# Performance work log

Hardware: AMD Instinct MI355X
Metric: run time of the kernel (lower is better)

Reference implementation:

```python
import jax, jax.numpy as jnp
import numpy as np

KS = 5          # B-spline kernel_size per pseudo-coordinate dim
DIM = 2         # pseudo-coordinate dimensionality
NUM_GRAPHS = 64


def spline_conv(x, src, dst, edge_attr, W, root, bias):
    """Degree-1 open B-spline conv (torch-spline-conv semantics, aggr='mean').
    x: [N,Cin], edge_attr: [E,DIM] in [0,1], W: [KS**DIM,Cin,Cout]."""
    N = x.shape[0]
    E = src.shape[0]
    v = edge_attr * (KS - 1)                                   # [E,DIM]
    k_lo = jnp.clip(jnp.floor(v), 0, KS - 2).astype(jnp.int32) # lower knot index
    frac = v - k_lo.astype(v.dtype)                            # [E,DIM]
    # Precompute x @ W_k for all K kernel weights per node: [N,K,Cout]
    xW = jnp.einsum('nc,kco->nko', x, W)
    msg = jnp.zeros((E, W.shape[2]), x.dtype)
    # 2^DIM = 4 nonzero basis products for degree-1 splines
    for bits in ((0, 0), (0, 1), (1, 0), (1, 1)):
        b = jnp.ones((E,), x.dtype)
        wi = jnp.zeros((E,), jnp.int32)
        stride = 1
        for d, bit in enumerate(bits):
            b = b * (frac[:, d] if bit else (1.0 - frac[:, d]))
            wi = wi + (k_lo[:, d] + bit) * stride
            stride *= KS
        msg = msg + b[:, None] * xW[src, wi]                   # gather [E,Cout]
    agg = jax.ops.segment_sum(msg, dst, num_segments=N)
    deg = jax.ops.segment_sum(jnp.ones((E,), x.dtype), dst, num_segments=N)
    agg = agg / jnp.maximum(deg, 1.0)[:, None]                 # mean aggregation
    return agg + x @ root + bias


def setup_inputs() -> dict:
    key = jax.random.key(0)
    ks = jax.random.split(key, 12)
    N, E = 20000, 320000
    Cin, H, O = 1, 32, 10
    K = KS * KS
    p = lambda k, s: jax.random.normal(k, s, jnp.float32) * 0.1
    return {
        'x': jax.random.normal(ks[0], (N, Cin), jnp.float32),
        'edge_attr': jax.random.uniform(ks[1], (E, DIM), jnp.float32),
        'W1': p(ks[2], (K, Cin, H)), 'root1': p(ks[3], (Cin, H)), 'b1': jnp.zeros((H,), jnp.float32),
        'W2': p(ks[4], (K, H, 2 * H)), 'root2': p(ks[5], (H, 2 * H)), 'b2': jnp.zeros((2 * H,), jnp.float32),
        'Wf1': p(ks[6], (2 * H, 128)), 'bf1': jnp.zeros((128,), jnp.float32),
        'Wf2': p(ks[7], (128, O)), 'bf2': jnp.zeros((O,), jnp.float32),
        'edge_index': jax.random.randint(ks[8], (2, E), 0, N),
        'batch': jnp.sort(jax.random.randint(ks[9], (N,), 0, NUM_GRAPHS)),
    }


def reference(x, edge_attr, W1, root1, b1, W2, root2, b2, Wf1, bf1, Wf2, bf2, edge_index, batch):
    src, dst = edge_index[0], edge_index[1]
    h = jax.nn.relu(spline_conv(x, src, dst, edge_attr, W1, root1, b1))
    h = jax.nn.relu(spline_conv(h, src, dst, edge_attr, W2, root2, b2))
    # global mean pool over graphs
    gsum = jax.ops.segment_sum(h, batch, num_segments=NUM_GRAPHS)
    cnt = jax.ops.segment_sum(jnp.ones((h.shape[0],), h.dtype), batch, num_segments=NUM_GRAPHS)
    g = gsum / jnp.maximum(cnt, 1.0)[:, None]
    g = jax.nn.relu(g @ Wf1 + bf1)
    return jax.nn.log_softmax(g @ Wf2 + bf2, axis=1)
```

## Files before the change

kernel.cpp:

```cpp
#include <hip/hip_runtime.h>
#include <hip/hip_fp16.h>
#include <math.h>

#define KK 25
#define H1C 32
#define H2C 64
#define FCC 128
#define NCLS 10
#define NG 64
#define M1 16
#define M2 10
#define TILEU 12800

typedef _Float16 v8h __attribute__((ext_vector_type(8)));
typedef _Float16 v4h __attribute__((ext_vector_type(4)));
typedef float v4f __attribute__((ext_vector_type(4)));

__global__ __launch_bounds__(256) void deg_kernel(
    const int* __restrict__ edge_index, int E,
    int* __restrict__ degi,
    const float* __restrict__ W2, __half* __restrict__ W2t) {
    int i = blockIdx.x * 256 + threadIdx.x;
    if (i < KK * H2C * H1C) {
        int c = i & 31, o = (i >> 5) & 63, k = i >> 11;
        W2t[i] = __float2half(W2[(k * H1C + c) * H2C + o]);
    }
    if (i < E) atomicAdd(&degi[edge_index[E + i]], 1);
}

__global__ void scan1_kernel(const int* __restrict__ degi, int N,
                             int* __restrict__ incl, int* __restrict__ bsum) {
    __shared__ int s[256];
    int tid = threadIdx.x;
    int i = blockIdx.x * 256 + tid;
    int v = (i < N) ? degi[i] : 0;
    s[tid] = v;
    __syncthreads();
    for (int off = 1; off < 256; off <<= 1) {
        int t = (tid >= off) ? s[tid - off] : 0;
        __syncthreads();
        s[tid] += t;
        __syncthreads();
    }
    if (i < N) incl[i] = s[tid];
    if (tid == 255) bsum[blockIdx.x] = s[255];
}

__global__ void scan23_kernel(const int* __restrict__ incl, const int* __restrict__ degi,
                              const int* __restrict__ bsum, int nb, int N,
                              int* __restrict__ rowst, int* __restrict__ cur) {
    __shared__ int s[256];
    int tid = threadIdx.x;
    int lim = min(nb, (int)blockIdx.x);
    int v = 0;
    for (int j = tid; j < lim; j += 256) v += bsum[j];
    s[tid] = v;
    __syncthreads();
    for (int off = 1; off < 256; off <<= 1) {
        int t = (tid >= off) ? s[tid - off] : 0;
        __syncthreads();
        s[tid] += t;
        __syncthreads();
    }
    int prior = s[255];
    int i = blockIdx.x * 256 + tid;
    if (i < N) {
        int r = incl[i] - degi[i] + prior;
        rowst[i] = r;
        cur[i] = r;
    }
}

__global__ void bucket_kernel(const float* __restrict__ edge_attr,
                              const int* __restrict__ edge_index, int E,
                              int* __restrict__ cur, int4* __restrict__ es) {
    int e = blockIdx.x * blockDim.x + threadIdx.x;
    if (e >= E) return;
    float v0 = edge_attr[2 * e + 0] * 4.0f;
    float v1 = edge_attr[2 * e + 1] * 4.0f;
    int k0 = (int)floorf(v0); k0 = min(max(k0, 0), 3);
    int k1 = (int)floorf(v1); k1 = min(max(k1, 0), 3);
    float f0 = v0 - (float)k0, f1 = v1 - (float)k1;
    int dst = edge_index[E + e];
    int pos = atomicAdd(&cur[dst], 1);
    es[pos] = make_int4(edge_index[e], (dst << 8) | (k0 + 5 * k1),
                        __float_as_int(f0), __float_as_int(f1));
}

__global__ __launch_bounds__(256) void l1_kernel(
    const float* __restrict__ x,
    const int* __restrict__ rowst, const int* __restrict__ degi,
    const int4* __restrict__ es,
    const float* __restrict__ W1, const float* __restrict__ root1,
    const float* __restrict__ b1,
    const __half* __restrict__ W2t,
    int N, int E,
    float* __restrict__ h1, __half* __restrict__ xph) {
    __shared__ float w1s[KK * H1C];
    __shared__ float agg1[M1 * H1C];
    __shared__ int4 eb[8][32];
    __shared__ float xb[8][32];
    __shared__ __half h1s[M1][H1C];
    __shared__ __half stg[5][M1][68];
    int tid = threadIdx.x;
    for (int i = tid; i < KK * H1C; i += 256) w1s[i] = W1[i];
    for (int i = tid; i < M1 * H1C; i += 256) agg1[i] = 0.0f;
    __syncthreads();
    int g = tid >> 5, o = tid & 31;
    int n0 = blockIdx.x * M1;
    int blkBeg = rowst[n0];
    int blkEnd = (n0 + M1 < N) ? rowst[n0 + M1] : E;
    int total = blkEnd - blkBeg;
    int per = (total + 7) >> 3;
    int wBeg = blkBeg + g * per;
    int wEnd = min(blkEnd, wBeg + per);
    int curDst = -1;
    float acc = 0.0f;
    for (int base = wBeg; base < wEnd; base += 32) {
        int m = min(32, wEnd - base);
        if (o < m) {
            int4 ed = es[base + o];
            eb[g][o] = ed;
            xb[g][o] = x[ed.x];
        }
        for (int j = 0; j < m; j++) {
            int4 ed = eb[g][j];
            float xs = xb[g][j];
            int dst = ed.y >> 8;
            if (dst != curDst) {
                if (curDst >= 0) atomicAdd(&agg1[(curDst - n0) * H1C + o], acc);
                acc = 0.0f;
                curDst = dst;
            }
            float f0 = __int_as_float(ed.z), f1 = __int_as_float(ed.w);
            float g0 = 1.0f - f0, g1 = 1.0f - f1;
            int kb = (ed.y & 0xff) << 5;
            float coef = g0 * g1 * w1s[kb + o] + f0 * g1 * w1s[kb + 32 + o] +
                         g0 * f1 * w1s[kb + 160 + o] + f0 * f1 * w1s[kb + 192 + o];
            acc = fmaf(xs, coef, acc);
        }
    }
    if (curDst >= 0) atomicAdd(&agg1[(curDst - n0) * H1C + o], acc);
    __syncthreads();
#pragma unroll
    for (int i = 0; i < 2; i++) {
        int ln = g + 8 * i;
        int n = n0 + ln;
        if (n < N) {
            float rdeg = 1.0f / fmaxf((float)degi[n], 1.0f);
            float hv = fmaxf(agg1[ln * H1C + o] * rdeg + x[n] * root1[o] + b1[o], 0.0f);
            h1[n * H1C + o] = hv;
            h1s[ln][o] = __float2half(hv);
        } else {
            h1s[ln][o] = __float2half(0.0f);
        }
    }
    __syncthreads();

    int w = tid >> 6, lane = tid & 63;
    int r15 = lane & 15, quad = lane >> 4;
    int o0 = w * 16;
    v8h bfrag = *(const v8h*)(&h1s[r15][quad * 8]);
    __half* xtile = xph + (size_t)blockIdx.x * (2 * TILEU);
    int cln = tid >> 4, coc = (tid & 15) * 4;
    bool crow = (n0 + cln) < N;
    for (int kc = 0; kc < KK; kc += 5) {
#pragma unroll
        for (int kk = 0; kk < 5; kk++) {
            int k = kc + kk;
            v8h afrag = *(const v8h*)(W2t + ((k << 6) + o0 + r15) * H1C + quad * 8);
            v4f acc2 = {};
            acc2 = __builtin_amdgcn_mfma_f32_16x16x32_f16(afrag, bfrag, acc2, 0, 0, 0);
            v4h hv;
            hv[0] = (_Float16)acc2[0];
            hv[1] = (_Float16)acc2[1];
            hv[2] = (_Float16)acc2[2];
            hv[3] = (_Float16)acc2[3];
            *(v4h*)(&stg[kk][r15][o0 + quad * 4]) = hv;
        }
        __syncthreads();
#pragma unroll
        for (int kk = 0; kk < 5; kk++) {
            if (crow) {
                v4h hv = *(const v4h*)(&stg[kk][cln][coc]);
                *(v4h*)(xtile + ((kc + kk) << 10) + (tid << 2)) = hv;
            }
        }
        __syncthreads();
    }
}

__global__ __launch_bounds__(256) void l2_kernel(
    const float* __restrict__ h1,
    const int* __restrict__ rowst, const int* __restrict__ degi,
    const int4* __restrict__ es,
    const unsigned* __restrict__ xphu,
    const float* __restrict__ root2, const float* __restrict__ b2,
    const int* __restrict__ batch,
    int N, int E, float* __restrict__ gsum) {
    __shared__ float agg[M2 * H2C];
    __shared__ int4 eb[4][64];
    int tid = threadIdx.x;
    for (int i = tid; i < M2 * H2C; i += 256) agg[i] = 0.0f;
    __syncthreads();
    int w = tid >> 6, lane = tid & 63;
    int o2 = lane & 31, eh = lane >> 5;
    int n0 = blockIdx.x * M2;
    int blkBeg = rowst[n0];
    int blkEnd = (n0 + M2 < N) ? rowst[n0 + M2] : E;
    int total = blkEnd - blkBeg;
    int per = (total + 3) >> 2;
    int wBeg = blkBeg + w * per;
    int wEnd = min(blkEnd, wBeg + per);
    int curDst = -1;
    float ax = 0.0f, ay = 0.0f;
    for (int base = wBeg; base < wEnd; base += 64) {
        int m = min(64, wEnd - base);
        if (lane < m) eb[w][lane] = es[base + lane];
        for (int j = 0; j < m; j += 2) {
            int jj = j + eh;
            bool act = jj < m;
            int4 ed = eb[w][act ? jj : j];
            const unsigned* p = xphu + (size_t)(ed.x >> 4) * TILEU +
                                ((ed.y & 0xff) << 9) + ((ed.x & 15) << 5) + o2;
            unsigned t0 = p[0], t1 = p[512], t2 = p[2560], t3 = p[3072];
            if (act) {
                int dst = ed.y >> 8;
                if (dst != curDst) {
                    if (curDst >= 0) {
                        atomicAdd(&agg[(curDst - n0) * H2C + 2 * o2], ax);
                        atomicAdd(&agg[(curDst - n0) * H2C + 2 * o2 + 1], ay);
                    }
                    ax = ay = 0.0f;
                    curDst = dst;
                }
                float f0 = __int_as_float(ed.z), f1 = __int_as_float(ed.w);
                float g0 = 1.0f - f0, g1 = 1.0f - f1;
                float b0 = g0 * g1, b1 = f0 * g1, bb2 = g0 * f1, b3 = f0 * f1;
                __half2 h0 = *(__half2*)&t0, h1v = *(__half2*)&t1;
                __half2 h2 = *(__half2*)&t2, h3 = *(__half2*)&t3;
                ax = fmaf(b0, __low2float(h0), ax);  ay = fmaf(b0, __high2float(h0), ay);
                ax = fmaf(b1, __low2float(h1v), ax); ay = fmaf(b1, __high2float(h1v), ay);
                ax = fmaf(bb2, __low2float(h2), ax); ay = fmaf(bb2, __high2float(h2), ay);
                ax = fmaf(b3, __low2float(h3), ax);  ay = fmaf(b3, __high2float(h3), ay);
            }
        }
    }
    if (curDst >= 0) {
        atomicAdd(&agg[(curDst - n0) * H2C + 2 * o2], ax);
        atomicAdd(&agg[(curDst - n0) * H2C + 2 * o2 + 1], ay);
    }
    __syncthreads();

#pragma unroll
    for (int i = 0; i < 3; i++) {
        int ln = w + 4 * i;
        int n = n0 + ln;
        if (ln < M2) {
            if (n < N) {
                float rd = 1.0f / fmaxf((float)degi[n], 1.0f);
                float v = agg[ln * H2C + lane] * rd + b2[lane];
                const float* hr = h1 + n * H1C;
#pragma unroll 8
                for (int c = 0; c < H1C; c++) v = fmaf(hr[c], root2[c * H2C + lane], v);
                agg[ln * H2C + lane] = fmaxf(v, 0.0f);
            } else {
                agg[ln * H2C + lane] = 0.0f;
            }
        }
    }
    __syncthreads();

    if (tid < H2C) {
        float run = 0.0f;
        int curg = batch[n0];
        for (int ln = 0; ln < M2; ln++) {
            int n = n0 + ln;
            if (n >= N) break;
            int gg = batch[n];
            if (gg != curg) {
                atomicAdd(&gsum[curg * H2C + tid], run);
                run = 0.0f;
                curg = gg;
            }
            run += agg[ln * H2C + tid];
        }
        atomicAdd(&gsum[curg * H2C + tid], run);
    }
}

__global__ void head_kernel(const float* __restrict__ gsum,
                            const int* __restrict__ batch, int N,
                            const float* __restrict__ Wf1, const float* __restrict__ bf1,
                            const float* __restrict__ Wf2, const float* __restrict__ bf2,
                            float* __restrict__ out) {
    __shared__ float gc[H2C];
    __shared__ float t1[FCC];
    __shared__ float lg[NCLS];
    __shared__ float lse;
    __shared__ float scnt;
    int g = blockIdx.x, tid = threadIdx.x;
    if (tid == 0) {
        int lo = 0, hi = N;
        while (lo < hi) { int m = (lo + hi) >> 1; if (batch[m] < g) lo = m + 1; else hi = m; }
        int lb = lo;
        lo = 0; hi = N;
        while (lo < hi) { int m = (lo + hi) >> 1; if (batch[m] <= g) lo = m + 1; else hi = m; }
        scnt = (float)(lo - lb);
    }
    __syncthreads();
    if (tid < H2C) gc[tid] = gsum[g * H2C + tid] / fmaxf(scnt, 1.0f);
    __syncthreads();
    {
        float acc = bf1[tid];
        for (int c = 0; c < H2C; c++) acc += gc[c] * Wf1[c * FCC + tid];
        t1[tid] = fmaxf(acc, 0.0f);
    }
    __syncthreads();
    if (tid < NCLS) {
        float acc = bf2[tid];
        for (int j = 0; j < FCC; j++) acc += t1[j] * Wf2[j * NCLS + tid];
        lg[tid] = acc;
    }
    __syncthreads();
    if (tid == 0) {
        float m = lg[0];
        for (int c = 1; c < NCLS; c++) m = fmaxf(m, lg[c]);
        float s = 0.0f;
        for (int c = 0; c < NCLS; c++) s += expf(lg[c] - m);
        lse = m + logf(s);
    }
    __syncthreads();
    if (tid < NCLS) out[g * NCLS + tid] = lg[tid] - lse;
}

extern "C" void kernel_launch(void* const* d_in, const int* in_sizes, int n_in,
                              void* d_out, int out_size, void* d_ws, size_t ws_size,
                              hipStream_t stream) {
    const float* x          = (const float*)d_in[0];
    const float* edge_attr  = (const float*)d_in[1];
    const float* W1         = (const float*)d_in[2];
    const float* root1      = (const float*)d_in[3];
    const float* b1         = (const float*)d_in[4];
    const float* W2         = (const float*)d_in[5];
    const float* root2      = (const float*)d_in[6];
    const float* b2         = (const float*)d_in[7];
    const float* Wf1        = (const float*)d_in[8];
    const float* bf1        = (const float*)d_in[9];
    const float* Wf2        = (const float*)d_in[10];
    const float* bf2        = (const float*)d_in[11];
    const int*   edge_index = (const int*)d_in[12];
    const int*   batch      = (const int*)d_in[13];
    float* out = (float*)d_out;

    const int N = in_sizes[13];
    const int E = in_sizes[12] / 2;
    const int NB = (N + 255) / 256;
    const int NT1 = (N + M1 - 1) / M1;

    int4*     es   = (int4*)d_ws;
    unsigned* xphu = (unsigned*)(es + E);
    __half*   w2t  = (__half*)(xphu + (size_t)NT1 * TILEU);
    float* gsum  = (float*)(w2t + KK * H2C * H1C);
    int*   degi  = (int*)(gsum + NG * H2C);
    int*   rowst = degi + N;
    int*   cur   = rowst + N;
    int*   incl  = cur + N;
    int*   bsum  = incl + N;
    float* h1    = (float*)(bsum + 256);

    hipMemsetAsync(gsum, 0, (size_t)NG * H2C * sizeof(float) + (size_t)N * sizeof(int),
                   stream);

    int degBlocks = (E + 255) / 256;
    deg_kernel<<<degBlocks, 256, 0, stream>>>(edge_index, E, degi, W2, w2t);

    scan1_kernel<<<NB, 256, 0, stream>>>(degi, N, incl, bsum);
    scan23_kernel<<<NB, 256, 0, stream>>>(incl, degi, bsum, NB, N, rowst, cur);

    bucket_kernel<<<(E + 255) / 256, 256, 0, stream>>>(edge_attr, edge_index, E, cur, es);

    l1_kernel<<<NT1, 256, 0, stream>>>(
        x, rowst, degi, es, W1, root1, b1, w2t, N, E, h1, (__half*)xphu);

    l2_kernel<<<(N + M2 - 1) / M2, 256, 0, stream>>>(
        h1, rowst, degi, es, xphu, root2, b2, batch, N, E, gsum);

    head_kernel<<<NG, FCC, 0, stream>>>(gsum, batch, N, Wf1, bf1, Wf2, bf2, out);
}
```

Baseline: 195.8 us.

## Fuse CSR preprocessing stages into one cooperative kernel with grid syncs

Replaces the memset, degree-count, two scan kernels and edge bucketing with a single cooperative launch of 512 blocks that uses grid-wide barriers between phases. The aim is to remove several kernel launch gaps and the separate memset. In exchange it adds four grid.sync barriers and grid-stride loops over fewer threads, and it relies on NB (79 blocks) fitting within 512 and on all 512 blocks being co-resident.

```diff
diff --git a/kernel.cpp b/kernel.cpp
--- a/kernel.cpp
+++ b/kernel.cpp
@@ -1,6 +1,9 @@
 #include <hip/hip_runtime.h>
 #include <hip/hip_fp16.h>
+#include <hip/hip_cooperative_groups.h>
 #include <math.h>
+
+namespace cg = cooperative_groups;
 
 #define KK 25
 #define H1C 32
@@ -11,80 +14,86 @@
 #define M1 16
 #define M2 10
 #define TILEU 12800
+#define PREPB 512
 
 typedef _Float16 v8h __attribute__((ext_vector_type(8)));
 typedef _Float16 v4h __attribute__((ext_vector_type(4)));
 typedef float v4f __attribute__((ext_vector_type(4)));
 
-__global__ __launch_bounds__(256) void deg_kernel(
-    const int* __restrict__ edge_index, int E,
+__global__ __launch_bounds__(256) void prep_kernel(
+    const int* __restrict__ edge_index, int E, int N, int NB,
     int* __restrict__ degi,
-    const float* __restrict__ W2, __half* __restrict__ W2t) {
-    int i = blockIdx.x * 256 + threadIdx.x;
-    if (i < KK * H2C * H1C) {
+    const float* __restrict__ W2, __half* __restrict__ W2t,
+    const float* __restrict__ edge_attr,
+    int* __restrict__ incl, int* __restrict__ bsum,
+    int* __restrict__ rowst, int* __restrict__ cur,
+    int4* __restrict__ es, float* __restrict__ gsum) {
+    cg::grid_group grid = cg::this_grid();
+    __shared__ int s[256];
+    int tid = threadIdx.x;
+    int gid = blockIdx.x * 256 + tid;
+    const int stride = PREPB * 256;
+
+    for (int i = gid; i < KK * H2C * H1C; i += stride) {
         int c = i & 31, o = (i >> 5) & 63, k = i >> 11;
         W2t[i] = __float2half(W2[(k * H1C + c) * H2C + o]);
     }
-    if (i < E) atomicAdd(&degi[edge_index[E + i]], 1);
-}
-
-__global__ void scan1_kernel(const int* __restrict__ degi, int N,
-                             int* __restrict__ incl, int* __restrict__ bsum) {
-    __shared__ int s[256];
-    int tid = threadIdx.x;
-    int i = blockIdx.x * 256 + tid;
-    int v = (i < N) ? degi[i] : 0;
-    s[tid] = v;
-    __syncthreads();
-    for (int off = 1; off < 256; off <<= 1) {
-        int t = (tid >= off) ? s[tid - off] : 0;
+    for (int i = gid; i < N; i += stride) degi[i] = 0;
+    for (int i = gid; i < NG * H2C; i += stride) gsum[i] = 0.0f;
+    grid.sync();
+
+    for (int e = gid; e < E; e += stride) atomicAdd(&degi[edge_index[E + e]], 1);
+    grid.sync();
+
+    if ((int)blockIdx.x < NB) {
+        int i = blockIdx.x * 256 + tid;
+        int v = (i < N) ? degi[i] : 0;
+        s[tid] = v;
         __syncthreads();
-        s[tid] += t;
+        for (int off = 1; off < 256; off <<= 1) {
+            int t = (tid >= off) ? s[tid - off] : 0;
+            __syncthreads();
+            s[tid] += t;
+            __syncthreads();
+        }
+        if (i < N) incl[i] = s[tid];
+        if (tid == 255) bsum[blockIdx.x] = s[255];
+    }
+    grid.sync();
+
+    if ((int)blockIdx.x < NB) {
+        int lim = min(NB, (int)blockIdx.x);
+        int v = 0;
+        for (int j = tid; j < lim; j += 256) v += bsum[j];
+        s[tid] = v;
         __syncthreads();
-    }
-    if (i < N) incl[i] = s[tid];
-    if (tid == 255) bsum[blockIdx.x] = s[255];
-}
-
-__global__ void scan23_kernel(const int* __restrict__ incl, const int* __restrict__ degi,
-                              const int* __restrict__ bsum, int nb, int N,
-                              int* __restrict__ rowst, int* __restrict__ cur) {
-    __shared__ int s[256];
-    int tid = threadIdx.x;
-    int lim = min(nb, (int)blockIdx.x);
-    int v = 0;
-    for (int j = tid; j < lim; j += 256) v += bsum[j];
-    s[tid] = v;
-    __syncthreads();
-    for (int off = 1; off < 256; off <<= 1) {
-        int t = (tid >= off) ? s[tid - off] : 0;
-        __syncthreads();
-        s[tid] += t;
-        __syncthreads();
-    }
-    int prior = s[255];
-    int i = blockIdx.x * 256 + tid;
-    if (i < N) {
-        int r = incl[i] - degi[i] + prior;
-        rowst[i] = r;
-        cur[i] = r;
-    }
-}
-
-__global__ void bucket_kernel(const float* __restrict__ edge_attr,
-                              const int* __restrict__ edge_index, int E,
-                              int* __restrict__ cur, int4* __restrict__ es) {
-    int e = blockIdx.x * blockDim.x + threadIdx.x;
-    if (e >= E) return;
-    float v0 = edge_attr[2 * e + 0] * 4.0f;
-    float v1 = edge_attr[2 * e + 1] * 4.0f;
-    int k0 = (int)floorf(v0); k0 = min(max(k0, 0), 3);
-    int k1 = (int)floorf(v1); k1 = min(max(k1, 0), 3);
-    float f0 = v0 - (float)k0, f1 = v1 - (float)k1;
-    int dst = edge_index[E + e];
-    int pos = atomicAdd(&cur[dst], 1);
-    es[pos] = make_int4(edge_index[e], (dst << 8) | (k0 + 5 * k1),
-                        __float_as_int(f0), __float_as_int(f1));
+        for (int off = 1; off < 256; off <<= 1) {
+            int t = (tid >= off) ? s[tid - off] : 0;
+            __syncthreads();
+            s[tid] += t;
+            __syncthreads();
+        }
+        int prior = s[255];
+        int i = blockIdx.x * 256 + tid;
+        if (i < N) {
+            int r = incl[i] - degi[i] + prior;
+            rowst[i] = r;
+            cur[i] = r;
+        }
+    }
+    grid.sync();
+
+    for (int e = gid; e < E; e += stride) {
+        float v0 = edge_attr[2 * e + 0] * 4.0f;
+        float v1 = edge_attr[2 * e + 1] * 4.0f;
+        int k0 = (int)floorf(v0); k0 = min(max(k0, 0), 3);
+        int k1 = (int)floorf(v1); k1 = min(max(k1, 0), 3);
+        float f0 = v0 - (float)k0, f1 = v1 - (float)k1;
+        int dst = edge_index[E + e];
+        int pos = atomicAdd(&cur[dst], 1);
+        es[pos] = make_int4(edge_index[e], (dst << 8) | (k0 + 5 * k1),
+                            __float_as_int(f0), __float_as_int(f1));
+    }
 }
 
 __global__ __launch_bounds__(256) void l1_kernel(
@@ -353,9 +362,9 @@
     const int*   batch      = (const int*)d_in[13];
     float* out = (float*)d_out;
 
-    const int N = in_sizes[13];
-    const int E = in_sizes[12] / 2;
-    const int NB = (N + 255) / 256;
+    int N = in_sizes[13];
+    int E = in_sizes[12] / 2;
+    int NB = (N + 255) / 256;
     const int NT1 = (N + M1 - 1) / M1;
 
     int4*     es   = (int4*)d_ws;
@@ -369,16 +378,20 @@
     int*   bsum  = incl + N;
     float* h1    = (float*)(bsum + 256);
 
-    hipMemsetAsync(gsum, 0, (size_t)NG * H2C * sizeof(float) + (size_t)N * sizeof(int),
-                   stream);
-
-    int degBlocks = (E + 255) / 256;
-    deg_kernel<<<degBlocks, 256, 0, stream>>>(edge_index, E, degi, W2, w2t);
-
-    scan1_kernel<<<NB, 256, 0, stream>>>(degi, N, incl, bsum);
-    scan23_kernel<<<NB, 256, 0, stream>>>(incl, degi, bsum, NB, N, rowst, cur);
-
-    bucket_kernel<<<(E + 255) / 256, 256, 0, stream>>>(edge_attr, edge_index, E, cur, es);
+    {
+        const int*   ei_p  = edge_index;
+        const float* W2_p  = W2;
+        __half*      w2t_p = w2t;
+        const float* ea_p  = edge_attr;
+        void* args[] = {
+            (void*)&ei_p, (void*)&E, (void*)&N, (void*)&NB,
+            (void*)&degi, (void*)&W2_p, (void*)&w2t_p, (void*)&ea_p,
+            (void*)&incl, (void*)&bsum, (void*)&rowst, (void*)&cur,
+            (void*)&es, (void*)&gsum
+        };
+        hipLaunchCooperativeKernel((const void*)prep_kernel, dim3(PREPB), dim3(256),
+                                   args, 0, stream);
+    }
 
     l1_kernel<<<NT1, 256, 0, stream>>>(
         x, rowst, degi, es, W1, root1, b1, w2t, N, E, h1, (__half*)xphu);
```

New measurement: 410.0 us. 2.09x slower.
